# Kernel optimization log

Hardware: AMD Instinct MI355X
Metric: run time of the kernel (lower is better)

Reference implementation:

```python
import math
import jax, jax.numpy as jnp
import numpy as np

N_TOKENS = 2048
HIDDEN = 2880
HEAD_DIM = 64
N_HEADS = 64          # total attention heads
N_KV = 8              # key/value heads
Q_MULT = N_HEADS // N_KV
SLIDING_WINDOW = 128  # layer_idx=0 (even) -> window active
ROPE_BASE = 150000.0
INIT_CTX = 4096.0
ROPE_SCALE = 32.0
NTK_ALPHA = 1.0
NTK_BETA = 32.0
QKV_DIM = HEAD_DIM * (N_HEADS + 2 * N_KV)  # 5120
EPS = 1e-5
NEG = -1e30


def _cos_sin(n_tokens):
    # YaRN-scaled rotary tables (scaling_factor > 1 branch)
    freq = ROPE_BASE ** (jnp.arange(0, HEAD_DIM, 2, dtype=jnp.float32) / HEAD_DIM)
    concentration = 0.1 * jnp.log(jnp.float32(ROPE_SCALE)) + 1.0
    d_half = HEAD_DIM / 2
    log_base = jnp.log(jnp.float32(ROPE_BASE))
    low = d_half * jnp.log(jnp.float32(INIT_CTX / (NTK_BETA * 2 * np.pi))) / log_base
    high = d_half * jnp.log(jnp.float32(INIT_CTX / (NTK_ALPHA * 2 * np.pi))) / log_base
    interpolation = 1.0 / (ROPE_SCALE * freq)
    extrapolation = 1.0 / freq
    ramp = (jnp.arange(d_half, dtype=jnp.float32) - low) / (high - low)
    mask = 1.0 - jnp.clip(ramp, 0.0, 1.0)
    inv_freq = interpolation * (1.0 - mask) + extrapolation * mask
    t = jnp.arange(n_tokens, dtype=jnp.float32)
    freqs = t[:, None] * inv_freq[None, :]          # [n, head_dim//2]
    return jnp.cos(freqs) * concentration, jnp.sin(freqs) * concentration


def _apply_rotary(x, cos, sin):
    # x: [n, heads, head_dim]; cos/sin: [n, head_dim//2]
    cos = cos[:, None, :].astype(x.dtype)
    sin = sin[:, None, :].astype(x.dtype)
    x1, x2 = jnp.split(x, 2, axis=-1)
    return jnp.concatenate((x1 * cos - x2 * sin, x2 * cos + x1 * sin), axis=-1)


def _rmsnorm(x, scale):
    t = x.astype(jnp.float32)
    rms = jnp.sqrt(jnp.mean(t * t, axis=-1, keepdims=True) + EPS)
    return (t / rms * scale).astype(x.dtype)


def _sdpa(q, k, v, sinks):
    # q: [n, h_kv, q_mult, d]; k, v: [n, h_kv, d]; sinks: [n_heads]
    n = q.shape[0]
    sm_scale = 1.0 / math.sqrt(HEAD_DIM)
    q32, k32, v32 = q.astype(jnp.float32), k.astype(jnp.float32), v.astype(jnp.float32)
    qk = jnp.einsum('qhmd,khd->hmqk', q32, k32) * jnp.float32(sm_scale)
    i = jnp.arange(n)
    # causal AND within sliding window: q - window < k <= q
    allowed = (i[None, :] <= i[:, None]) & (i[None, :] > i[:, None] - SLIDING_WINDOW)
    qk = qk + jnp.where(allowed, jnp.float32(0.0), jnp.float32(NEG))[None, None, :, :]
    s = sinks.astype(jnp.float32).reshape(N_KV, Q_MULT, 1, 1)
    s = jnp.broadcast_to(s, (N_KV, Q_MULT, n, 1))
    w = jax.nn.softmax(jnp.concatenate([qk, s], axis=-1), axis=-1)[..., :-1]
    attn = jnp.einsum('hmqk,khd->qhmd', w, v32)
    return attn.astype(q.dtype).reshape(n, -1)  # [n, n_heads*head_dim]


def setup_inputs() -> dict:
    key = jax.random.key(0)
    ks = jax.random.split(key, 5)
    s = 0.02
    return {
        'x': jax.random.normal(ks[0], (N_TOKENS, HIDDEN), jnp.float32),
        'norm_scale': jnp.ones((HIDDEN,), jnp.float32),
        'w_qkv': jax.random.normal(ks[1], (HIDDEN, QKV_DIM), jnp.float32) * s,
        'b_qkv': jnp.zeros((QKV_DIM,), jnp.float32),
        'sinks': jax.random.normal(ks[2], (N_HEADS,), jnp.float32),
        'w_out': jax.random.normal(ks[3], (N_HEADS * HEAD_DIM, HIDDEN), jnp.float32) * s,
        'b_out': jnp.zeros((HIDDEN,), jnp.float32),
    }


def reference(x, norm_scale, w_qkv, b_qkv, sinks, w_out, b_out):
    n = x.shape[0]
    t = _rmsnorm(x, norm_scale)
    qkv = t @ w_qkv + b_qkv                                   # [n, qkv_dim]
    q_end = N_HEADS * HEAD_DIM
    k_end = q_end + N_KV * HEAD_DIM
    q = qkv[:, :q_end].reshape(n, N_KV, Q_MULT, HEAD_DIM)
    k = qkv[:, q_end:k_end].reshape(n, N_KV, HEAD_DIM)
    v = qkv[:, k_end:].reshape(n, N_KV, HEAD_DIM)
    cos, sin = _cos_sin(n)
    q = _apply_rotary(q.reshape(n, -1, HEAD_DIM), cos, sin).reshape(n, N_KV, Q_MULT, HEAD_DIM)
    k = _apply_rotary(k, cos, sin)
    attn = _sdpa(q, k, v, sinks)                              # [n, n_heads*head_dim]
    return x + (attn @ w_out + b_out)
```

## Files before the change

### kernel.cpp

```cpp
#include <hip/hip_runtime.h>
#include <hip/hip_bf16.h>
#include <math.h>

#define N_TOK 2048
#define HIDDEN 2880
#define QKV_DIM 5120
#define LOG2E 1.44269504088896340736f

typedef __attribute__((ext_vector_type(8))) short short8;
typedef __attribute__((ext_vector_type(4))) float f32x4;
typedef __attribute__((ext_vector_type(16))) float f32x16;

__device__ __forceinline__ float bf2f(unsigned short u) {
  union { unsigned int i; float f; } c; c.i = ((unsigned int)u) << 16; return c.f;
}
__device__ __forceinline__ unsigned short f2bf(float f) {
  union { float f; unsigned int i; } c; c.f = f;
  unsigned int i = c.i;
  return (unsigned short)((i + 0x7FFFu + ((i >> 16) & 1u)) >> 16);
}
__device__ __forceinline__ void gload16(const void* g, void* l) {
  __builtin_amdgcn_global_load_lds((const __attribute__((address_space(1))) void*)g,
                                   (__attribute__((address_space(3))) void*)l, 16, 0, 0);
}

__global__ __launch_bounds__(256) void rmsnorm_kernel(
    const float* __restrict__ x, const float* __restrict__ scale,
    unsigned short* __restrict__ t)
{
  int row = blockIdx.x;
  const float* xr = x + (size_t)row * HIDDEN;
  float ss = 0.f;
  for (int i = threadIdx.x; i < HIDDEN / 4; i += 256) {
    float4 v = ((const float4*)xr)[i];
    ss += v.x * v.x + v.y * v.y + v.z * v.z + v.w * v.w;
  }
#pragma unroll
  for (int off = 32; off; off >>= 1) ss += __shfl_down(ss, off, 64);
  __shared__ float red[4];
  if ((threadIdx.x & 63) == 0) red[threadIdx.x >> 6] = ss;
  __syncthreads();
  float total = red[0] + red[1] + red[2] + red[3];
  float rinv = rsqrtf(total / (float)HIDDEN + 1e-5f);
  for (int i = threadIdx.x; i < HIDDEN / 4; i += 256) {
    float4 v = ((const float4*)xr)[i];
    float4 s4 = ((const float4*)scale)[i];
    union { unsigned short u[4]; uint2 p; } pk;
    pk.u[0] = f2bf(v.x * rinv * s4.x);
    pk.u[1] = f2bf(v.y * rinv * s4.y);
    pk.u[2] = f2bf(v.z * rinv * s4.z);
    pk.u[3] = f2bf(v.w * rinv * s4.w);
    *(uint2*)&t[(size_t)row * HIDDEN + i * 4] = pk.p;
  }
}

__global__ __launch_bounds__(256) void transpose_cast(
    const float* __restrict__ in, unsigned short* __restrict__ out,
    int R, int C, int outStride)
{
  __shared__ float tile[32][33];
  int c0 = blockIdx.x * 32, r0 = blockIdx.y * 32;
  int tx = threadIdx.x & 31, ty = threadIdx.x >> 5;
#pragma unroll
  for (int rr = ty; rr < 32; rr += 8)
    tile[rr][tx] = in[(size_t)(r0 + rr) * C + c0 + tx];
  __syncthreads();
#pragma unroll
  for (int rr = ty; rr < 32; rr += 8)
    out[(size_t)(c0 + rr) * outStride + r0 + tx] = f2bf(tile[tx][rr]);
}

template <int NF, int EPI>
__global__ __launch_bounds__(512, 2) void gemm8(
    const unsigned short* __restrict__ A,
    const unsigned short* __restrict__ Bt,
    const float* __restrict__ bias,
    const float* __restrict__ resid,
    void* __restrict__ Cout,
    int K, int Ncols)
{
  constexpr int BUFSZ = 16384 + NF * 8192;
  constexpr int NCH = 2 + NF;
  constexpr int HALF = NCH / 2;
  __shared__ char smem_[2 * BUFSZ];
  const int tid = threadIdx.x;
  const int lane = tid & 63;
  const int w = tid >> 6;
  const int fr = lane & 15, fq = lane >> 4;
  const int wr = w >> 2, wc = w & 3;

  const int nwg = gridDim.x;
  const int cpx = nwg >> 3;
  const int wg = (blockIdx.x & 7) * cpx + (blockIdx.x >> 3);
  const int by = wg & 15, bx = wg >> 4;
  const int row0 = by * 128, col0 = bx * (NF * 64);

  const unsigned short* gsrc[NCH];
  int ldsoff[NCH];
#pragma unroll
  for (int c = 0; c < NCH; ++c) {
    int g = tid + 512 * c;
    if (g < 1024) {
      int kk = g >> 9, rr = (g >> 2) & 127, u = g & 3;
      gsrc[c] = A + (size_t)(row0 + rr) * K + kk * 32 + ((u ^ ((rr >> 1) & 3)) * 8);
      ldsoff[c] = kk * 8192 + rr * 64 + u * 16;
    } else {
      int g2 = g - 1024;
      int kk = g2 / (NF * 256);
      int rm = g2 - kk * (NF * 256);
      int rr = rm >> 2, u = rm & 3;
      gsrc[c] = Bt + (size_t)(col0 + rr) * K + kk * 32 + ((u ^ ((rr >> 1) & 3)) * 8);
      ldsoff[c] = 16384 + kk * (NF * 4096) + rr * 64 + u * 16;
    }
  }
  const int urd = (fq ^ ((fr >> 1) & 3)) * 16;
  const int aoffb = (wr * 64 + fr) * 64 + urd;
  const int boffb = 16384 + (wc * NF * 16 + fr) * 64 + urd;

  f32x4 acc[4][NF];
#pragma unroll
  for (int mf = 0; mf < 4; ++mf)
#pragma unroll
    for (int nf = 0; nf < NF; ++nf) acc[mf][nf] = (f32x4)0.f;

  const int NT = K >> 6;

#define ISSUE(c) gload16(gsrc[c] + ktn, smem_ + nbufo + ldsoff[c])
#define RD_A(mf, kk) (*(const short8*)(smem_ + bufo + (kk)*8192 + (mf)*1024 + aoffb))
#define RD_B(nf, kk) (*(const short8*)(smem_ + bufo + (kk)*(NF*4096) + (nf)*1024 + boffb))

  {
    const int ktn = 0, nbufo = 0;
#pragma unroll
    for (int c = 0; c < NCH; ++c) gload16(gsrc[c] + ktn, smem_ + nbufo + ldsoff[c]);
  }

  for (int t = 0; t < NT; ++t) {
    const int bufo = (t & 1) * BUFSZ;
    const int nbufo = bufo ^ BUFSZ;
    const int ktn = (t + 1) * 64;
    const bool pref = (t + 1) < NT;

    asm volatile("s_waitcnt vmcnt(0)" ::: "memory");
    __builtin_amdgcn_s_barrier();

    if (pref) {
#pragma unroll
      for (int c = 0; c < HALF; ++c) ISSUE(c);
    }

    short8 afr[4], bfr[NF];
#pragma unroll
    for (int nf = 0; nf < NF; ++nf) bfr[nf] = RD_B(nf, 0);
#pragma unroll
    for (int mf = 0; mf < 4; ++mf) afr[mf] = RD_A(mf, 0);
    __builtin_amdgcn_s_setprio(1);
#pragma unroll
    for (int mf = 0; mf < 4; ++mf)
#pragma unroll
      for (int nf = 0; nf < NF; ++nf)
        acc[mf][nf] = __builtin_amdgcn_mfma_f32_16x16x32_bf16(afr[mf], bfr[nf], acc[mf][nf], 0, 0, 0);
    __builtin_amdgcn_s_setprio(0);

    if (pref) {
#pragma unroll
      for (int c = HALF; c < NCH; ++c) ISSUE(c);
    }

#pragma unroll
    for (int nf = 0; nf < NF; ++nf) bfr[nf] = RD_B(nf, 1);
#pragma unroll
    for (int mf = 0; mf < 4; ++mf) afr[mf] = RD_A(mf, 1);
    __builtin_amdgcn_s_setprio(1);
#pragma unroll
    for (int mf = 0; mf < 4; ++mf)
#pragma unroll
      for (int nf = 0; nf < NF; ++nf)
        acc[mf][nf] = __builtin_amdgcn_mfma_f32_16x16x32_bf16(afr[mf], bfr[nf], acc[mf][nf], 0, 0, 0);
    __builtin_amdgcn_s_setprio(0);
  }
#undef ISSUE
#undef RD_A
#undef RD_B

#pragma unroll
  for (int mf = 0; mf < 4; ++mf) {
#pragma unroll
    for (int nf = 0; nf < NF; ++nf) {
      const int colb = col0 + wc * NF * 16 + nf * 16 + fr;
      const int rowb = row0 + wr * 64 + mf * 16 + fq * 4;
      const float bs = bias[colb];
      if (EPI == 1) {
#pragma unroll
        for (int j = 0; j < 4; ++j)
          ((unsigned short*)Cout)[(size_t)(rowb + j) * Ncols + colb] =
              f2bf(acc[mf][nf][j] + bs);
      } else {
#pragma unroll
        for (int j = 0; j < 4; ++j) {
          const size_t idx = (size_t)(rowb + j) * Ncols + colb;
          ((float*)Cout)[idx] = acc[mf][nf][j] + bs + resid[idx];
        }
      }
    }
  }
}

__global__ __launch_bounds__(256) void rope_kernel(unsigned short* __restrict__ qkv)
{
  int token = blockIdx.y;
  int p = blockIdx.x * 256 + threadIdx.x;
  if (p >= 72 * 32) return;
  int h = p >> 5, j = p & 31;
  const float log_base = 11.9183905731f;
  float fj = (float)j;
  float extrap = expf(-log_base * fj * 0.03125f);
  float interp = extrap * 0.03125f;
  const float low  = 32.f * logf(4096.f / (32.f * 6.283185307179586f)) / log_base;
  const float high = 32.f * logf(4096.f / 6.283185307179586f) / log_base;
  float ramp = (fj - low) / (high - low);
  float maskv = 1.f - fminf(fmaxf(ramp, 0.f), 1.f);
  float inv_freq = interp * (1.f - maskv) + extrap * maskv;
  float ang = (float)token * inv_freq;
  const float conc = 1.3465735903f;
  float s, c;
  sincosf(ang, &s, &c);
  c *= conc; s *= conc;
  size_t base = (size_t)token * QKV_DIM + h * 64 + j;
  float x1 = bf2f(qkv[base]), x2 = bf2f(qkv[base + 32]);
  qkv[base]      = f2bf(x1 * c - x2 * s);
  qkv[base + 32] = f2bf(x2 * c + x1 * s);
}

__global__ __launch_bounds__(512) void attn_kernel(
    const unsigned short* __restrict__ qkv, const float* __restrict__ sinks,
    unsigned short* __restrict__ attn)
{
  __shared__ unsigned short Ks[160 * 64];
  __shared__ unsigned short Vt[64 * 192];
  const int tid  = threadIdx.x;
  const int lane = tid & 63;
  const int w    = tid >> 6;
  const int qb = blockIdx.x, kvh = blockIdx.y;
  const int q0 = qb * 32;
  const int kb = q0 - 128;
  const int h  = lane >> 5;
  const int ql = lane & 31;

  for (int it = w; it < 20; it += 8) {
    int r = it * 8 + (lane >> 3);
    int s = lane & 7;
    int j = kb + r; if (j < 0) j = 0;
    const unsigned short* src =
        qkv + (size_t)j * QKV_DIM + 4096 + kvh * 64 + ((s ^ (r & 7)) * 8);
    gload16(src, &Ks[r * 64 + s * 8]);
  }
  for (int c = tid; c < 2560; c += 512) {
    int jl = c >> 4;
    int d4 = (c & 15) * 4;
    int j = kb + jl; if (j < 0) j = 0;
    ushort4 v4 = *(const ushort4*)&qkv[(size_t)j * QKV_DIM + 4608 + kvh * 64 + d4];
    const unsigned short* pv = (const unsigned short*)&v4;
#pragma unroll
    for (int t = 0; t < 4; ++t) {
      int d = d4 + t;
      int slot = (jl >> 3) ^ (d & 7);
      Vt[d * 192 + slot * 8 + (jl & 7)] = pv[t];
    }
  }
  const int head = kvh * 8 + w;
  const int i_q = q0 + ql;
  short8 qf[4];
  {
    const unsigned short* qp = qkv + (size_t)i_q * QKV_DIM + head * 64 + h * 8;
#pragma unroll
    for (int ks = 0; ks < 4; ++ks) qf[ks] = *(const short8*)(qp + ks * 16);
  }
  __syncthreads();

  const float SC = 0.125f * LOG2E;
  f32x16 oacc0 = (f32x16)(0.f), oacc1 = (f32x16)(0.f);
  float m = -1e30f, l = 0.f;

  const int tstart = qb < 4 ? 4 - qb : 0;
  for (int tt = tstart; tt < 5; ++tt) {
    const int j0 = kb + tt * 32;
    f32x16 sacc = (f32x16)(0.f);
    const int kr = tt * 32 + ql;
#pragma unroll
    for (int ks = 0; ks < 4; ++ks) {
      short8 kf = *(const short8*)&Ks[kr * 64 + (((ks * 2 + h) ^ (kr & 7)) * 8)];
      sacc = __builtin_amdgcn_mfma_f32_32x32x16_bf16(kf, qf[ks], sacc, 0, 0, 0);
    }
    float sc16[16];
    float mt = -INFINITY;
#pragma unroll
    for (int e = 0; e < 16; ++e) {
      int kk = (e & 3) + 8 * (e >> 2) + 4 * h;
      int j = j0 + kk;
      float s2 = sacc[e] * SC;
      bool valid = (j <= i_q) && (j > i_q - 128);
      s2 = valid ? s2 : -INFINITY;
      sc16[e] = s2;
      mt = fmaxf(mt, s2);
    }
    mt = fmaxf(mt, __shfl_xor(mt, 32));
    float mnew = fmaxf(m, mt);
    float r = exp2f(m - mnew);
    l *= r;
    oacc0 *= r;
    oacc1 *= r;
    m = mnew;
    unsigned int wpk[8];
    float ls = 0.f;
#pragma unroll
    for (int e2 = 0; e2 < 8; ++e2) {
      float plo = exp2f(sc16[2 * e2]     - m);
      float phi = exp2f(sc16[2 * e2 + 1] - m);
      ls += plo + phi;
      asm("v_cvt_pk_bf16_f32 %0, %1, %2" : "=v"(wpk[e2]) : "v"(plo), "v"(phi));
    }
    l += ls;
#pragma unroll
    for (int m16 = 0; m16 < 2; ++m16) {
      int go = 2 * m16 + h;
      int gs = 2 * m16 + 1 - h;
      unsigned int x0 = (unsigned int)__shfl_xor((int)wpk[2 * gs],     32);
      unsigned int x1 = (unsigned int)__shfl_xor((int)wpk[2 * gs + 1], 32);
      union { unsigned int u[4]; short8 s; } bu;
      bu.u[0] = h ? x0 : wpk[2 * go];
      bu.u[1] = h ? x1 : wpk[2 * go + 1];
      bu.u[2] = h ? wpk[2 * go]     : x0;
      bu.u[3] = h ? wpk[2 * go + 1] : x1;
      short8 bfrag = bu.s;
#pragma unroll
      for (int dt = 0; dt < 2; ++dt) {
        int d = dt * 32 + ql;
        int slot = (tt * 4 + m16 * 2 + h) ^ (d & 7);
        short8 vf = *(const short8*)&Vt[d * 192 + slot * 8];
        if (dt == 0)
          oacc0 = __builtin_amdgcn_mfma_f32_32x32x16_bf16(vf, bfrag, oacc0, 0, 0, 0);
        else
          oacc1 = __builtin_amdgcn_mfma_f32_32x32x16_bf16(vf, bfrag, oacc1, 0, 0, 0);
      }
    }
  }
  float lt = l + __shfl_xor(l, 32);
  lt += exp2f(sinks[head] * LOG2E - m);
  float inv = 1.f / lt;
  unsigned short* op = attn + (size_t)i_q * 4096 + head * 64;
#pragma unroll
  for (int dt = 0; dt < 2; ++dt) {
#pragma unroll
    for (int g = 0; g < 4; ++g) {
      float f0, f1, f2, f3;
      if (dt == 0) {
        f0 = oacc0[4 * g]; f1 = oacc0[4 * g + 1]; f2 = oacc0[4 * g + 2]; f3 = oacc0[4 * g + 3];
      } else {
        f0 = oacc1[4 * g]; f1 = oacc1[4 * g + 1]; f2 = oacc1[4 * g + 2]; f3 = oacc1[4 * g + 3];
      }
      unsigned int u0, u1;
      asm("v_cvt_pk_bf16_f32 %0, %1, %2" : "=v"(u0) : "v"(f0 * inv), "v"(f1 * inv));
      asm("v_cvt_pk_bf16_f32 %0, %1, %2" : "=v"(u1) : "v"(f2 * inv), "v"(f3 * inv));
      int d = dt * 32 + 8 * g + 4 * h;
      uint2 pr; pr.x = u0; pr.y = u1;
      *(uint2*)(op + d) = pr;
    }
  }
}

extern "C" void kernel_launch(void* const* d_in, const int* in_sizes, int n_in,
                              void* d_out, int out_size, void* d_ws, size_t ws_size,
                              hipStream_t stream)
{
  const float* x      = (const float*)d_in[0];
  const float* nscale = (const float*)d_in[1];
  const float* w_qkv  = (const float*)d_in[2];
  const float* b_qkv  = (const float*)d_in[3];
  const float* sinks  = (const float*)d_in[4];
  const float* w_out  = (const float*)d_in[5];
  const float* b_out  = (const float*)d_in[6];

  char* ws = (char*)d_ws;
  unsigned short* t_bf  = (unsigned short*)(ws);
  unsigned short* wqkvT = (unsigned short*)(ws + 11796480);
  unsigned short* qkv   = (unsigned short*)(ws + 41287680);
  unsigned short* attn  = (unsigned short*)(ws + 62259200);
  unsigned short* woutT = (unsigned short*)(ws + 79036416);

  rmsnorm_kernel<<<N_TOK, 256, 0, stream>>>(x, nscale, t_bf);
  transpose_cast<<<dim3(5120 / 32, 2880 / 32), 256, 0, stream>>>(w_qkv, wqkvT, 2880, 5120, 2880);
  transpose_cast<<<dim3(2880 / 32, 4096 / 32), 256, 0, stream>>>(w_out, woutT, 4096, 2880, 4096);
  gemm8<5, 1><<<256, 512, 0, stream>>>(t_bf, wqkvT, b_qkv, nullptr, (void*)qkv, 2880, 5120);
  rope_kernel<<<dim3(9, N_TOK), 256, 0, stream>>>(qkv);
  attn_kernel<<<dim3(64, 8), 512, 0, stream>>>(qkv, sinks, attn);
  gemm8<3, 2><<<240, 512, 0, stream>>>(attn, woutT, b_out, x, d_out, 4096, 2880);
}
```

Baseline: 203.4 us.

## Triple-buffer B tiles with two-step prefetch and partial vmcnt waits in GEMM

Reorganizes the GEMM shared-memory pipeline: the A tile stays double-buffered while the B tile gets three buffers and is prefetched two k-steps ahead. The per-iteration wait changes from a full vmcnt(0) drain to a partial wait that lets the newer B loads stay in flight. All prefetches are now issued right after the barrier instead of being split around the first MFMA half. This is meant to hide global-load latency better, at the cost of more LDS, which may reduce occupancy for larger NF.

Result: no change. 206.1 us (+1.3%).

```diff
diff --git a/kernel.cpp b/kernel.cpp
--- a/kernel.cpp
+++ b/kernel.cpp
@@ -79,10 +79,8 @@
     void* __restrict__ Cout,
     int K, int Ncols)
 {
-  constexpr int BUFSZ = 16384 + NF * 8192;
-  constexpr int NCH = 2 + NF;
-  constexpr int HALF = NCH / 2;
-  __shared__ char smem_[2 * BUFSZ];
+  constexpr int BSZ = NF * 8192;
+  __shared__ char smem_[32768 + 3 * BSZ];
   const int tid = threadIdx.x;
   const int lane = tid & 63;
   const int w = tid >> 6;
@@ -95,27 +93,29 @@
   const int by = wg & 15, bx = wg >> 4;
   const int row0 = by * 128, col0 = bx * (NF * 64);
 
-  const unsigned short* gsrc[NCH];
-  int ldsoff[NCH];
-#pragma unroll
-  for (int c = 0; c < NCH; ++c) {
+  const unsigned short* gsrcA[2];
+  int ldsoffA[2];
+#pragma unroll
+  for (int c = 0; c < 2; ++c) {
     int g = tid + 512 * c;
-    if (g < 1024) {
-      int kk = g >> 9, rr = (g >> 2) & 127, u = g & 3;
-      gsrc[c] = A + (size_t)(row0 + rr) * K + kk * 32 + ((u ^ ((rr >> 1) & 3)) * 8);
-      ldsoff[c] = kk * 8192 + rr * 64 + u * 16;
-    } else {
-      int g2 = g - 1024;
-      int kk = g2 / (NF * 256);
-      int rm = g2 - kk * (NF * 256);
-      int rr = rm >> 2, u = rm & 3;
-      gsrc[c] = Bt + (size_t)(col0 + rr) * K + kk * 32 + ((u ^ ((rr >> 1) & 3)) * 8);
-      ldsoff[c] = 16384 + kk * (NF * 4096) + rr * 64 + u * 16;
-    }
+    int kk = g >> 9, rr = (g >> 2) & 127, u = g & 3;
+    gsrcA[c] = A + (size_t)(row0 + rr) * K + kk * 32 + ((u ^ ((rr >> 1) & 3)) * 8);
+    ldsoffA[c] = kk * 8192 + rr * 64 + u * 16;
+  }
+  const unsigned short* gsrcB[NF];
+  int ldsoffB[NF];
+#pragma unroll
+  for (int c = 0; c < NF; ++c) {
+    int g = tid + 512 * c;
+    int kk = g / (NF * 256);
+    int rm = g - kk * (NF * 256);
+    int rr = rm >> 2, u = rm & 3;
+    gsrcB[c] = Bt + (size_t)(col0 + rr) * K + kk * 32 + ((u ^ ((rr >> 1) & 3)) * 8);
+    ldsoffB[c] = kk * (NF * 4096) + rr * 64 + u * 16;
   }
   const int urd = (fq ^ ((fr >> 1) & 3)) * 16;
   const int aoffb = (wr * 64 + fr) * 64 + urd;
-  const int boffb = 16384 + (wc * NF * 16 + fr) * 64 + urd;
+  const int boffb = (wc * NF * 16 + fr) * 64 + urd;
 
   f32x4 acc[4][NF];
 #pragma unroll
@@ -125,28 +125,41 @@
 
   const int NT = K >> 6;
 
-#define ISSUE(c) gload16(gsrc[c] + ktn, smem_ + nbufo + ldsoff[c])
-#define RD_A(mf, kk) (*(const short8*)(smem_ + bufo + (kk)*8192 + (mf)*1024 + aoffb))
-#define RD_B(nf, kk) (*(const short8*)(smem_ + bufo + (kk)*(NF*4096) + (nf)*1024 + boffb))
-
-  {
-    const int ktn = 0, nbufo = 0;
-#pragma unroll
-    for (int c = 0; c < NCH; ++c) gload16(gsrc[c] + ktn, smem_ + nbufo + ldsoff[c]);
-  }
-
+#define RD_A(mf, kk) (*(const short8*)(smem_ + abase + (kk)*8192 + (mf)*1024 + aoffb))
+#define RD_B(nf, kk) (*(const short8*)(smem_ + bbase + (kk)*(NF*4096) + (nf)*1024 + boffb))
+
+#pragma unroll
+  for (int c = 0; c < 2; ++c) gload16(gsrcA[c], smem_ + ldsoffA[c]);
+#pragma unroll
+  for (int c = 0; c < NF; ++c) gload16(gsrcB[c], smem_ + 32768 + ldsoffB[c]);
+#pragma unroll
+  for (int c = 0; c < NF; ++c) gload16(gsrcB[c] + 64, smem_ + 32768 + BSZ + ldsoffB[c]);
+
+  int bCur = 0;
   for (int t = 0; t < NT; ++t) {
-    const int bufo = (t & 1) * BUFSZ;
-    const int nbufo = bufo ^ BUFSZ;
-    const int ktn = (t + 1) * 64;
-    const bool pref = (t + 1) < NT;
-
-    asm volatile("s_waitcnt vmcnt(0)" ::: "memory");
+    const int abase = (t & 1) * 16384;
+    const int bbase = 32768 + bCur * BSZ;
+
+    if (t < NT - 1) {
+      if constexpr (NF == 5) asm volatile("s_waitcnt vmcnt(5)" ::: "memory");
+      else                   asm volatile("s_waitcnt vmcnt(3)" ::: "memory");
+    } else {
+      asm volatile("s_waitcnt vmcnt(0)" ::: "memory");
+    }
     __builtin_amdgcn_s_barrier();
 
-    if (pref) {
-#pragma unroll
-      for (int c = 0; c < HALF; ++c) ISSUE(c);
+    if (t + 1 < NT) {
+      const int ktn = (t + 1) * 64;
+      const int an = (abase ^ 16384);
+#pragma unroll
+      for (int c = 0; c < 2; ++c) gload16(gsrcA[c] + ktn, smem_ + an + ldsoffA[c]);
+    }
+    if (t + 2 < NT) {
+      const int ktn2 = (t + 2) * 64;
+      int b2 = bCur + 2; if (b2 >= 3) b2 -= 3;
+      const int bn = 32768 + b2 * BSZ;
+#pragma unroll
+      for (int c = 0; c < NF; ++c) gload16(gsrcB[c] + ktn2, smem_ + bn + ldsoffB[c]);
     }
 
     short8 afr[4], bfr[NF];
@@ -162,11 +175,6 @@
         acc[mf][nf] = __builtin_amdgcn_mfma_f32_16x16x32_bf16(afr[mf], bfr[nf], acc[mf][nf], 0, 0, 0);
     __builtin_amdgcn_s_setprio(0);
 
-    if (pref) {
-#pragma unroll
-      for (int c = HALF; c < NCH; ++c) ISSUE(c);
-    }
-
 #pragma unroll
     for (int nf = 0; nf < NF; ++nf) bfr[nf] = RD_B(nf, 1);
 #pragma unroll
@@ -178,8 +186,9 @@
       for (int nf = 0; nf < NF; ++nf)
         acc[mf][nf] = __builtin_amdgcn_mfma_f32_16x16x32_bf16(afr[mf], bfr[nf], acc[mf][nf], 0, 0, 0);
     __builtin_amdgcn_s_setprio(0);
-  }
-#undef ISSUE
+
+    bCur = (bCur + 1 == 3) ? 0 : bCur + 1;
+  }
 #undef RD_A
 #undef RD_B
 
```
